# Kernel optimization log

Measured on AMD Instinct MI355X. Metric: run time of the kernel, lower is better.

## Reference

```python
import jax, jax.numpy as jnp
import numpy as np

B, S, H = 32, 1024, 1024

def setup_inputs() -> dict:
    key = jax.random.key(0)
    k1, k2, k3, k4, k5 = jax.random.split(key, 5)
    scale = 1.0 / np.sqrt(H)
    return {
        "decoder_hidden": jax.random.normal(k1, (B, H), jnp.float32),
        "encoder_outputs": jax.random.normal(k2, (B, S, H), jnp.float32),
        "U_w": jax.random.normal(k3, (H, H), jnp.float32) * scale,
        "W_w": jax.random.normal(k4, (H, H), jnp.float32) * scale,
        "v_w": jax.random.normal(k5, (H,), jnp.float32) * scale,
    }

def reference(decoder_hidden, encoder_outputs, U_w, W_w, v_w):
    # U(decoder_hidden): [B, H] @ [H, H]^T -> [B, H], broadcast over S
    U_h = jnp.einsum('bh,oh->bo', decoder_hidden, U_w)          # [B, H]
    W_s = jnp.einsum('bsh,oh->bso', encoder_outputs, W_w)       # [B, S, H]
    # v(tanh(U_h + W_s)) -> attention scores [B, S]
    att = jnp.einsum('bsh,h->bs', jnp.tanh(U_h[:, None, :] + W_s), v_w)
    alpha = jax.nn.softmax(att, axis=1)                          # [B, S]
    context = jnp.einsum('bs,bsh->bh', alpha, encoder_outputs)   # [B, H]
    return (context, alpha)
```

## Files before the change

### kernel.cpp

```cpp
#include <hip/hip_runtime.h>
#include <hip/hip_bf16.h>
#include <cstdint>
#include <cstddef>

#define B_DIM 32
#define S_DIM 1024
#define H_DIM 1024
#define M_DIM (B_DIM * S_DIM)

typedef __attribute__((ext_vector_type(8))) short bf16x8;
typedef __attribute__((ext_vector_type(4))) float f32x4;

static __device__ __forceinline__ unsigned short f2bf(float f) {
  unsigned u = __float_as_uint(f);
  u = (u + 0x7FFFu + ((u >> 16) & 1u)) >> 16;
  return (unsigned short)u;
}
static __device__ __forceinline__ float bf2f(unsigned short u) {
  return __uint_as_float(((unsigned)u) << 16);
}
static __device__ __forceinline__ float fast_tanh(float x) {
  return 1.f - 2.f / (__expf(2.f * x) + 1.f);
}

static __device__ __forceinline__ void gload16(const unsigned short* g, char* l) {
  __builtin_amdgcn_global_load_lds(
      (const __attribute__((address_space(1))) unsigned int*)g,
      (__attribute__((address_space(3))) unsigned int*)l, 16, 0, 0);
}

__global__ void k_prep_all(const float* __restrict__ E, unsigned short* __restrict__ Eb,
                           const float* __restrict__ W, unsigned short* __restrict__ Wb,
                           const float* __restrict__ dh, const float* __restrict__ Uw,
                           float* __restrict__ Uh) {
  const int bid = blockIdx.x;
  if (bid < 2048) {
    const int n8 = M_DIM * (H_DIM / 8);
    const int stride = 2048 * 256;
    for (int idx = bid * 256 + threadIdx.x; idx < n8; idx += stride) {
      const float4* gp = (const float4*)(E + (size_t)idx * 8);
      float4 lo = gp[0], hi = gp[1];
      bf16x8 w;
      w[0] = (short)f2bf(lo.x); w[1] = (short)f2bf(lo.y);
      w[2] = (short)f2bf(lo.z); w[3] = (short)f2bf(lo.w);
      w[4] = (short)f2bf(hi.x); w[5] = (short)f2bf(hi.y);
      w[6] = (short)f2bf(hi.z); w[7] = (short)f2bf(hi.w);
      *(bf16x8*)(Eb + (size_t)idx * 8) = w;
    }
  } else if (bid < 3072) {
    const int idx = (bid - 2048) * 256 + threadIdx.x;
    float4 v = ((const float4*)W)[idx];
    ushort4 o;
    o.x = f2bf(v.x); o.y = f2bf(v.y); o.z = f2bf(v.z); o.w = f2bf(v.w);
    ((ushort4*)Wb)[idx] = o;
  } else {
    const int wave = threadIdx.x >> 6;
    const int lane = threadIdx.x & 63;
    const int o = (bid - 3072) * 4 + wave;
    float uw[16];
#pragma unroll
    for (int k = 0; k < 16; ++k) uw[k] = Uw[o * H_DIM + k * 64 + lane];
    for (int b = 0; b < B_DIM; ++b) {
      float acc = 0.f;
#pragma unroll
      for (int k = 0; k < 16; ++k) acc += uw[k] * dh[b * H_DIM + k * 64 + lane];
#pragma unroll
      for (int msk = 32; msk >= 1; msk >>= 1) acc += __shfl_xor(acc, msk, 64);
      if (lane == 0) Uh[b * H_DIM + o] = acc;
    }
  }
}

#define A5_BM 256
#define A5_BN 256
#define A5_BUF 65536
#define NT_FAST 4

__launch_bounds__(512, 2)
__global__ void k_att6(const unsigned short* __restrict__ Eb,
                       const unsigned short* __restrict__ Wb,
                       const float* __restrict__ Uh,
                       const float* __restrict__ vw,
                       float* __restrict__ att_p) {
  __shared__ __align__(16) char lds[2 * A5_BUF];

  const int bid = blockIdx.x;
  const int xj = bid & 7;
  const int q  = bid >> 3;
  const int n_tile = q & 3;
  const int m_tile = ((q >> 2) << 3) | xj;
  const int m0 = m_tile * A5_BM;
  const int n0 = n_tile * A5_BN;
  const int b  = m0 >> 10;

  const int tid  = threadIdx.x;
  const int wid  = tid >> 6;
  const int lane = tid & 63;
  const int wm = (wid >> 2) * 128;
  const int wn = (wid & 3) * 64;

  size_t offA[4], offB[4];
  int ldsA[4], ldsB[4];
#pragma unroll
  for (int j = 0; j < 4; ++j) {
    const int chunk = j * 512 + tid;
    const int r  = chunk >> 3;
    const int c8 = (chunk & 7) ^ (r & 7);
    offA[j] = (size_t)(m0 + r) * H_DIM + c8 * 8;
    offB[j] = (size_t)(n0 + r) * H_DIM + c8 * 8;
    ldsA[j] = j * 8192 + wid * 1024;
    ldsB[j] = 32768 + j * 8192 + wid * 1024;
  }

  auto stage = [&](int t) {
    char* dst = lds + (t & 1) * A5_BUF;
    const size_t k0 = (size_t)t * 64;
#pragma unroll
    for (int j = 0; j < 4; ++j) gload16(Eb + offA[j] + k0, dst + ldsA[j]);
#pragma unroll
    for (int j = 0; j < 4; ++j) gload16(Wb + offB[j] + k0, dst + ldsB[j]);
  };

  const int fr_row = lane & 15;
  const int fr_k8  = lane >> 4;

  f32x4 acc[8][4];
#pragma unroll
  for (int mf = 0; mf < 8; ++mf)
#pragma unroll
    for (int nf = 0; nf < 4; ++nf) acc[mf][nf] = (f32x4)(0.0f);

  stage(0);

  for (int t = 0; t < 16; ++t) {
    asm volatile("s_waitcnt vmcnt(0)" ::: "memory");
    __builtin_amdgcn_s_barrier();
    asm volatile("" ::: "memory");

    if (t < 15) stage(t + 1);

    const char* As = lds + (t & 1) * A5_BUF;
    const char* Bs = As + 32768;

#pragma unroll
    for (int kh = 0; kh < 2; ++kh) {
      const int kb = kh * 32 + fr_k8 * 8;
      bf16x8 af[8], bfr[4];
#pragma unroll
      for (int mf = 0; mf < 8; ++mf) {
        const int row = wm + mf * 16 + fr_row;
        const int addr = (row * 128 + kb * 2) ^ ((row & 7) << 4);
        af[mf] = *(const bf16x8*)(As + addr);
      }
#pragma unroll
      for (int nf = 0; nf < 4; ++nf) {
        const int row = wn + nf * 16 + fr_row;
        const int addr = (row * 128 + kb * 2) ^ ((row & 7) << 4);
        bfr[nf] = *(const bf16x8*)(Bs + addr);
      }
      __builtin_amdgcn_s_setprio(1);
#pragma unroll
      for (int mf = 0; mf < 8; ++mf)
#pragma unroll
        for (int nf = 0; nf < 4; ++nf)
          acc[mf][nf] = __builtin_amdgcn_mfma_f32_16x16x32_bf16(af[mf], bfr[nf], acc[mf][nf], 0, 0, 0);
      __builtin_amdgcn_s_setprio(0);
    }
  }

  float* red = (float*)lds;

  const int col = lane & 15;
  const int rhi = lane >> 4;
  float uh[4], vv[4];
#pragma unroll
  for (int nf = 0; nf < 4; ++nf) {
    const int o = n0 + wn + nf * 16 + col;
    uh[nf] = Uh[b * H_DIM + o];
    vv[nf] = vw[o];
  }
#pragma unroll
  for (int mf = 0; mf < 8; ++mf) {
    float rs[4];
#pragma unroll
    for (int jj = 0; jj < 4; ++jj) {
      float s = 0.f;
#pragma unroll
      for (int nf = 0; nf < 4; ++nf) {
        const float x = acc[mf][nf][jj] + uh[nf];
        s += fast_tanh(x) * vv[nf];
      }
      rs[jj] = s;
    }
#pragma unroll
    for (int msk = 1; msk < 16; msk <<= 1) {
#pragma unroll
      for (int jj = 0; jj < 4; ++jj) rs[jj] += __shfl_xor(rs[jj], msk, 64);
    }
    if (col == 0) {
#pragma unroll
      for (int jj = 0; jj < 4; ++jj) {
        const int local = mf * 16 + rhi * 4 + jj;
        red[wid * 128 + local] = rs[jj];
      }
    }
  }
  __syncthreads();
  if (tid < 256) {
    const int mhalf = tid >> 7;
    const int loc = tid & 127;
    float sum = 0.f;
#pragma unroll
    for (int j = 0; j < 4; ++j) sum += red[(mhalf * 4 + j) * 128 + loc];
    att_p[(size_t)n_tile * M_DIM + m0 + tid] = sum;
  }
}

__global__ void k_ctx_sm(const unsigned short* __restrict__ Eb,
                         const float* __restrict__ att_p,
                         float* __restrict__ alpha_out,
                         float* __restrict__ ctx_p) {
  const int bid = blockIdx.x;
  const int b  = bid >> 2;
  const int sq = bid & 3;
  const int tid = threadIdx.x;
  __shared__ float red[8];
  __shared__ float qa[256];

  float a[4];
  float mx = -1e30f;
#pragma unroll
  for (int i = 0; i < 4; ++i) {
    const int s = i * 256 + tid;
    float v = 0.f;
#pragma unroll
    for (int t = 0; t < NT_FAST; ++t) v += att_p[(size_t)t * M_DIM + b * S_DIM + s];
    a[i] = v;
    mx = fmaxf(mx, v);
  }
#pragma unroll
  for (int msk = 32; msk >= 1; msk >>= 1) mx = fmaxf(mx, __shfl_xor(mx, msk, 64));
  if ((tid & 63) == 0) red[tid >> 6] = mx;
  __syncthreads();
  mx = fmaxf(fmaxf(red[0], red[1]), fmaxf(red[2], red[3]));
  float sum = 0.f;
#pragma unroll
  for (int i = 0; i < 4; ++i) { a[i] = __expf(a[i] - mx); sum += a[i]; }
#pragma unroll
  for (int msk = 32; msk >= 1; msk >>= 1) sum += __shfl_xor(sum, msk, 64);
  if ((tid & 63) == 0) red[4 + (tid >> 6)] = sum;
  __syncthreads();
  const float inv = 1.f / (red[4] + red[5] + red[6] + red[7]);
  if (sq == 0) {
#pragma unroll
    for (int i = 0; i < 4; ++i) alpha_out[b * S_DIM + i * 256 + tid] = a[i] * inv;
  }
  qa[tid] = a[sq] * inv;
  __syncthreads();

  const int h = tid * 4;
  const unsigned short* ep = Eb + (size_t)b * S_DIM * H_DIM + (size_t)(sq * 256) * H_DIM + h;
  float4 acc = make_float4(0.f, 0.f, 0.f, 0.f);
  for (int s = 0; s < 256; ++s) {
    const float al = qa[s];
    ushort4 v = *(const ushort4*)(ep + (size_t)s * H_DIM);
    acc.x += al * bf2f(v.x);
    acc.y += al * bf2f(v.y);
    acc.z += al * bf2f(v.z);
    acc.w += al * bf2f(v.w);
  }
  *(float4*)&ctx_p[(size_t)sq * (B_DIM * H_DIM) + b * H_DIM + h] = acc;
}

__global__ void k_ctx_reduce(const float* __restrict__ ctx_p, float* __restrict__ ctx) {
  const int i = blockIdx.x * 256 + threadIdx.x;
  ctx[i] = ctx_p[i] + ctx_p[32768 + i] + ctx_p[65536 + i] + ctx_p[98304 + i];
}

extern "C" void kernel_launch(void* const* d_in, const int* in_sizes, int n_in,
                              void* d_out, int out_size, void* d_ws, size_t ws_size,
                              hipStream_t stream) {
  (void)in_sizes; (void)n_in; (void)out_size; (void)ws_size;
  const float* dh  = (const float*)d_in[0];
  const float* enc = (const float*)d_in[1];
  const float* Uw  = (const float*)d_in[2];
  const float* Ww  = (const float*)d_in[3];
  const float* vw  = (const float*)d_in[4];
  float* ctx_out = (float*)d_out;
  float* alpha   = (float*)d_out + M_DIM;

  char* ws = (char*)d_ws;
  const size_t EB_BYTES = (size_t)M_DIM * H_DIM * 2;

  unsigned short* Eb = (unsigned short*)ws;
  unsigned short* Wb = (unsigned short*)(ws + EB_BYTES);
  float* Uh    = (float*)(ws + EB_BYTES + (2u << 20));
  float* att_p = (float*)(ws + EB_BYTES + (2u << 20) + (128u << 10));
  float* ctx_p = (float*)(ws + EB_BYTES + (2u << 20) + (128u << 10) + (1u << 20));

  k_prep_all<<<3328, 256, 0, stream>>>(enc, Eb, Ww, Wb, dh, Uw, Uh);
  k_att6<<<512, 512, 0, stream>>>(Eb, Wb, Uh, vw, att_p);
  k_ctx_sm<<<128, 256, 0, stream>>>(Eb, att_p, alpha, ctx_p);
  k_ctx_reduce<<<128, 256, 0, stream>>>(ctx_p, ctx_out);
}
```

Before: 139.8 us.

## Interleave GEMM K-loop into four barrier-separated phases and rebalance prep blocks

```diff
diff --git a/kernel.cpp b/kernel.cpp
--- a/kernel.cpp
+++ b/kernel.cpp
@@ -34,10 +34,33 @@
                            const float* __restrict__ dh, const float* __restrict__ Uw,
                            float* __restrict__ Uh) {
   const int bid = blockIdx.x;
-  if (bid < 2048) {
+  if (bid < 1024) {
+    const int wave = threadIdx.x >> 6;
+    const int lane = threadIdx.x & 63;
+    const int o = bid;
+    float uw[16];
+#pragma unroll
+    for (int k = 0; k < 16; ++k) uw[k] = Uw[o * H_DIM + k * 64 + lane];
+#pragma unroll
+    for (int bb = 0; bb < 8; ++bb) {
+      const int b = wave * 8 + bb;
+      float acc = 0.f;
+#pragma unroll
+      for (int k = 0; k < 16; ++k) acc += uw[k] * dh[b * H_DIM + k * 64 + lane];
+#pragma unroll
+      for (int msk = 32; msk >= 1; msk >>= 1) acc += __shfl_xor(acc, msk, 64);
+      if (lane == 0) Uh[b * H_DIM + o] = acc;
+    }
+  } else if (bid < 2048) {
+    const int idx = (bid - 1024) * 256 + threadIdx.x;
+    float4 v = ((const float4*)W)[idx];
+    ushort4 o;
+    o.x = f2bf(v.x); o.y = f2bf(v.y); o.z = f2bf(v.z); o.w = f2bf(v.w);
+    ((ushort4*)Wb)[idx] = o;
+  } else {
     const int n8 = M_DIM * (H_DIM / 8);
     const int stride = 2048 * 256;
-    for (int idx = bid * 256 + threadIdx.x; idx < n8; idx += stride) {
+    for (int idx = (bid - 2048) * 256 + threadIdx.x; idx < n8; idx += stride) {
       const float4* gp = (const float4*)(E + (size_t)idx * 8);
       float4 lo = gp[0], hi = gp[1];
       bf16x8 w;
@@ -47,27 +70,6 @@
       w[6] = (short)f2bf(hi.z); w[7] = (short)f2bf(hi.w);
       *(bf16x8*)(Eb + (size_t)idx * 8) = w;
     }
-  } else if (bid < 3072) {
-    const int idx = (bid - 2048) * 256 + threadIdx.x;
-    float4 v = ((const float4*)W)[idx];
-    ushort4 o;
-    o.x = f2bf(v.x); o.y = f2bf(v.y); o.z = f2bf(v.z); o.w = f2bf(v.w);
-    ((ushort4*)Wb)[idx] = o;
-  } else {
-    const int wave = threadIdx.x >> 6;
-    const int lane = threadIdx.x & 63;
-    const int o = (bid - 3072) * 4 + wave;
-    float uw[16];
-#pragma unroll
-    for (int k = 0; k < 16; ++k) uw[k] = Uw[o * H_DIM + k * 64 + lane];
-    for (int b = 0; b < B_DIM; ++b) {
-      float acc = 0.f;
-#pragma unroll
-      for (int k = 0; k < 16; ++k) acc += uw[k] * dh[b * H_DIM + k * 64 + lane];
-#pragma unroll
-      for (int msk = 32; msk >= 1; msk >>= 1) acc += __shfl_xor(acc, msk, 64);
-      if (lane == 0) Uh[b * H_DIM + o] = acc;
-    }
   }
 }
 
@@ -76,8 +78,11 @@
 #define A5_BUF 65536
 #define NT_FAST 4
 
+#define LDFRAG(base, row, kh) \
+  (*(const bf16x8*)((base) + ((((row) * 128) + ((kh) * 32 + fr_k8 * 8) * 2) ^ (((row) & 7) << 4))))
+
 __launch_bounds__(512, 2)
-__global__ void k_att6(const unsigned short* __restrict__ Eb,
+__global__ void k_att7(const unsigned short* __restrict__ Eb,
                        const unsigned short* __restrict__ Wb,
                        const float* __restrict__ Uh,
                        const float* __restrict__ vw,
@@ -112,15 +117,6 @@
     ldsB[j] = 32768 + j * 8192 + wid * 1024;
   }
 
-  auto stage = [&](int t) {
-    char* dst = lds + (t & 1) * A5_BUF;
-    const size_t k0 = (size_t)t * 64;
-#pragma unroll
-    for (int j = 0; j < 4; ++j) gload16(Eb + offA[j] + k0, dst + ldsA[j]);
-#pragma unroll
-    for (int j = 0; j < 4; ++j) gload16(Wb + offB[j] + k0, dst + ldsB[j]);
-  };
-
   const int fr_row = lane & 15;
   const int fr_k8  = lane >> 4;
 
@@ -130,42 +126,115 @@
 #pragma unroll
     for (int nf = 0; nf < 4; ++nf) acc[mf][nf] = (f32x4)(0.0f);
 
-  stage(0);
+  {
+    char* dst = lds;
+#pragma unroll
+    for (int j = 0; j < 4; ++j) gload16(Eb + offA[j], dst + ldsA[j]);
+#pragma unroll
+    for (int j = 0; j < 4; ++j) gload16(Wb + offB[j], dst + ldsB[j]);
+  }
 
   for (int t = 0; t < 16; ++t) {
     asm volatile("s_waitcnt vmcnt(0)" ::: "memory");
     __builtin_amdgcn_s_barrier();
     asm volatile("" ::: "memory");
 
-    if (t < 15) stage(t + 1);
-
     const char* As = lds + (t & 1) * A5_BUF;
     const char* Bs = As + 32768;
-
-#pragma unroll
-    for (int kh = 0; kh < 2; ++kh) {
-      const int kb = kh * 32 + fr_k8 * 8;
-      bf16x8 af[8], bfr[4];
-#pragma unroll
-      for (int mf = 0; mf < 8; ++mf) {
-        const int row = wm + mf * 16 + fr_row;
-        const int addr = (row * 128 + kb * 2) ^ ((row & 7) << 4);
-        af[mf] = *(const bf16x8*)(As + addr);
-      }
-#pragma unroll
-      for (int nf = 0; nf < 4; ++nf) {
-        const int row = wn + nf * 16 + fr_row;
-        const int addr = (row * 128 + kb * 2) ^ ((row & 7) << 4);
-        bfr[nf] = *(const bf16x8*)(Bs + addr);
-      }
-      __builtin_amdgcn_s_setprio(1);
-#pragma unroll
-      for (int mf = 0; mf < 8; ++mf)
-#pragma unroll
-        for (int nf = 0; nf < 4; ++nf)
-          acc[mf][nf] = __builtin_amdgcn_mfma_f32_16x16x32_bf16(af[mf], bfr[nf], acc[mf][nf], 0, 0, 0);
-      __builtin_amdgcn_s_setprio(0);
-    }
+    char* dst = lds + ((t + 1) & 1) * A5_BUF;
+    const size_t k1 = (size_t)(t + 1) * 64;
+    const bool st = (t < 15);
+
+    bf16x8 afl[8], afh[8], b01[4], b23[4], b01b[4];
+
+#pragma unroll
+    for (int mf = 0; mf < 4; ++mf) {
+      afl[mf * 2 + 0] = LDFRAG(As, wm + mf * 16 + fr_row, 0);
+      afl[mf * 2 + 1] = LDFRAG(As, wm + mf * 16 + fr_row, 1);
+    }
+#pragma unroll
+    for (int nf = 0; nf < 2; ++nf) {
+      b01[nf * 2 + 0] = LDFRAG(Bs, wn + nf * 16 + fr_row, 0);
+      b01[nf * 2 + 1] = LDFRAG(Bs, wn + nf * 16 + fr_row, 1);
+    }
+    if (st) { gload16(Eb + offA[0] + k1, dst + ldsA[0]);
+              gload16(Eb + offA[1] + k1, dst + ldsA[1]); }
+    __builtin_amdgcn_s_barrier();
+    asm volatile("s_waitcnt lgkmcnt(0)" ::: "memory");
+    __builtin_amdgcn_sched_barrier(0);
+    __builtin_amdgcn_s_setprio(1);
+#pragma unroll
+    for (int mf = 0; mf < 4; ++mf)
+#pragma unroll
+      for (int nf = 0; nf < 2; ++nf) {
+        acc[mf][nf] = __builtin_amdgcn_mfma_f32_16x16x32_bf16(afl[mf*2+0], b01[nf*2+0], acc[mf][nf], 0, 0, 0);
+        acc[mf][nf] = __builtin_amdgcn_mfma_f32_16x16x32_bf16(afl[mf*2+1], b01[nf*2+1], acc[mf][nf], 0, 0, 0);
+      }
+    __builtin_amdgcn_s_setprio(0);
+    __builtin_amdgcn_s_barrier();
+
+#pragma unroll
+    for (int nf = 0; nf < 2; ++nf) {
+      b23[nf * 2 + 0] = LDFRAG(Bs, wn + (nf + 2) * 16 + fr_row, 0);
+      b23[nf * 2 + 1] = LDFRAG(Bs, wn + (nf + 2) * 16 + fr_row, 1);
+    }
+    if (st) { gload16(Eb + offA[2] + k1, dst + ldsA[2]);
+              gload16(Eb + offA[3] + k1, dst + ldsA[3]); }
+    __builtin_amdgcn_s_barrier();
+    asm volatile("s_waitcnt lgkmcnt(0)" ::: "memory");
+    __builtin_amdgcn_sched_barrier(0);
+    __builtin_amdgcn_s_setprio(1);
+#pragma unroll
+    for (int mf = 0; mf < 4; ++mf)
+#pragma unroll
+      for (int nf = 0; nf < 2; ++nf) {
+        acc[mf][nf+2] = __builtin_amdgcn_mfma_f32_16x16x32_bf16(afl[mf*2+0], b23[nf*2+0], acc[mf][nf+2], 0, 0, 0);
+        acc[mf][nf+2] = __builtin_amdgcn_mfma_f32_16x16x32_bf16(afl[mf*2+1], b23[nf*2+1], acc[mf][nf+2], 0, 0, 0);
+      }
+    __builtin_amdgcn_s_setprio(0);
+    __builtin_amdgcn_s_barrier();
+
+#pragma unroll
+    for (int mf = 0; mf < 4; ++mf) {
+      afh[mf * 2 + 0] = LDFRAG(As, wm + (mf + 4) * 16 + fr_row, 0);
+      afh[mf * 2 + 1] = LDFRAG(As, wm + (mf + 4) * 16 + fr_row, 1);
+    }
+    if (st) { gload16(Wb + offB[0] + k1, dst + ldsB[0]);
+              gload16(Wb + offB[1] + k1, dst + ldsB[1]); }
+    __builtin_amdgcn_s_barrier();
+    asm volatile("s_waitcnt lgkmcnt(0)" ::: "memory");
+    __builtin_amdgcn_sched_barrier(0);
+    __builtin_amdgcn_s_setprio(1);
+#pragma unroll
+    for (int mf = 0; mf < 4; ++mf)
+#pragma unroll
+      for (int nf = 0; nf < 2; ++nf) {
+        acc[mf+4][nf+2] = __builtin_amdgcn_mfma_f32_16x16x32_bf16(afh[mf*2+0], b23[nf*2+0], acc[mf+4][nf+2], 0, 0, 0);
+        acc[mf+4][nf+2] = __builtin_amdgcn_mfma_f32_16x16x32_bf16(afh[mf*2+1], b23[nf*2+1], acc[mf+4][nf+2], 0, 0, 0);
+      }
+    __builtin_amdgcn_s_setprio(0);
+    __builtin_amdgcn_s_barrier();
+
+#pragma unroll
+    for (int nf = 0; nf < 2; ++nf) {
+      b01b[nf * 2 + 0] = LDFRAG(Bs, wn + nf * 16 + fr_row, 0);
+      b01b[nf * 2 + 1] = LDFRAG(Bs, wn + nf * 16 + fr_row, 1);
+    }
+    if (st) { gload16(Wb + offB[2] + k1, dst + ldsB[2]);
+              gload16(Wb + offB[3] + k1, dst + ldsB[3]); }
+    __builtin_amdgcn_s_barrier();
+    asm volatile("s_waitcnt lgkmcnt(0)" ::: "memory");
+    __builtin_amdgcn_sched_barrier(0);
+    __builtin_amdgcn_s_setprio(1);
+#pragma unroll
+    for (int mf = 0; mf < 4; ++mf)
+#pragma unroll
+      for (int nf = 0; nf < 2; ++nf) {
+        acc[mf+4][nf] = __builtin_amdgcn_mfma_f32_16x16x32_bf16(afh[mf*2+0], b01b[nf*2+0], acc[mf+4][nf], 0, 0, 0);
+        acc[mf+4][nf] = __builtin_amdgcn_mfma_f32_16x16x32_bf16(afh[mf*2+1], b01b[nf*2+1], acc[mf+4][nf], 0, 0, 0);
+      }
+    __builtin_amdgcn_s_setprio(0);
+    __builtin_amdgcn_s_barrier();
   }
 
   float* red = (float*)lds;
@@ -298,8 +367,8 @@
   float* att_p = (float*)(ws + EB_BYTES + (2u << 20) + (128u << 10));
   float* ctx_p = (float*)(ws + EB_BYTES + (2u << 20) + (128u << 10) + (1u << 20));
 
-  k_prep_all<<<3328, 256, 0, stream>>>(enc, Eb, Ww, Wb, dh, Uw, Uh);
-  k_att6<<<512, 512, 0, stream>>>(Eb, Wb, Uh, vw, att_p);
+  k_prep_all<<<4096, 256, 0, stream>>>(enc, Eb, Ww, Wb, dh, Uw, Uh);
+  k_att7<<<512, 512, 0, stream>>>(Eb, Wb, Uh, vw, att_p);
   k_ctx_sm<<<128, 256, 0, stream>>>(Eb, att_p, alpha, ctx_p);
   k_ctx_reduce<<<128, 256, 0, stream>>>(ctx_p, ctx_out);
 }
```

Result: faster. 132.6 us (-5.1%).

## Shrink GEMM tiles to 128x256 with k32 stages and reorder prep blocks

Applied to the files above, without the earlier changes.

```diff
diff --git a/kernel.cpp b/kernel.cpp
--- a/kernel.cpp
+++ b/kernel.cpp
@@ -34,10 +34,33 @@
                            const float* __restrict__ dh, const float* __restrict__ Uw,
                            float* __restrict__ Uh) {
   const int bid = blockIdx.x;
-  if (bid < 2048) {
+  if (bid < 1024) {
+    const int wave = threadIdx.x >> 6;
+    const int lane = threadIdx.x & 63;
+    const int o = bid;
+    float uw[16];
+#pragma unroll
+    for (int k = 0; k < 16; ++k) uw[k] = Uw[o * H_DIM + k * 64 + lane];
+#pragma unroll
+    for (int bb = 0; bb < 8; ++bb) {
+      const int b = wave * 8 + bb;
+      float acc = 0.f;
+#pragma unroll
+      for (int k = 0; k < 16; ++k) acc += uw[k] * dh[b * H_DIM + k * 64 + lane];
+#pragma unroll
+      for (int msk = 32; msk >= 1; msk >>= 1) acc += __shfl_xor(acc, msk, 64);
+      if (lane == 0) Uh[b * H_DIM + o] = acc;
+    }
+  } else if (bid < 2048) {
+    const int idx = (bid - 1024) * 256 + threadIdx.x;
+    float4 v = ((const float4*)W)[idx];
+    ushort4 o;
+    o.x = f2bf(v.x); o.y = f2bf(v.y); o.z = f2bf(v.z); o.w = f2bf(v.w);
+    ((ushort4*)Wb)[idx] = o;
+  } else {
     const int n8 = M_DIM * (H_DIM / 8);
     const int stride = 2048 * 256;
-    for (int idx = bid * 256 + threadIdx.x; idx < n8; idx += stride) {
+    for (int idx = (bid - 2048) * 256 + threadIdx.x; idx < n8; idx += stride) {
       const float4* gp = (const float4*)(E + (size_t)idx * 8);
       float4 lo = gp[0], hi = gp[1];
       bf16x8 w;
@@ -47,125 +70,99 @@
       w[6] = (short)f2bf(hi.z); w[7] = (short)f2bf(hi.w);
       *(bf16x8*)(Eb + (size_t)idx * 8) = w;
     }
-  } else if (bid < 3072) {
-    const int idx = (bid - 2048) * 256 + threadIdx.x;
-    float4 v = ((const float4*)W)[idx];
-    ushort4 o;
-    o.x = f2bf(v.x); o.y = f2bf(v.y); o.z = f2bf(v.z); o.w = f2bf(v.w);
-    ((ushort4*)Wb)[idx] = o;
-  } else {
-    const int wave = threadIdx.x >> 6;
-    const int lane = threadIdx.x & 63;
-    const int o = (bid - 3072) * 4 + wave;
-    float uw[16];
-#pragma unroll
-    for (int k = 0; k < 16; ++k) uw[k] = Uw[o * H_DIM + k * 64 + lane];
-    for (int b = 0; b < B_DIM; ++b) {
-      float acc = 0.f;
-#pragma unroll
-      for (int k = 0; k < 16; ++k) acc += uw[k] * dh[b * H_DIM + k * 64 + lane];
-#pragma unroll
-      for (int msk = 32; msk >= 1; msk >>= 1) acc += __shfl_xor(acc, msk, 64);
-      if (lane == 0) Uh[b * H_DIM + o] = acc;
-    }
-  }
-}
-
-#define A5_BM 256
-#define A5_BN 256
-#define A5_BUF 65536
+  }
+}
+
+#define A8_BM 128
+#define A8_BN 256
+#define A8_BUF 24576
 #define NT_FAST 4
 
-__launch_bounds__(512, 2)
-__global__ void k_att6(const unsigned short* __restrict__ Eb,
+#define LDFRAG32(base, row) \
+  (*(const bf16x8*)((base) + (((row) * 64 + fr_k8 * 16) ^ (((row) & 3) << 4))))
+
+__launch_bounds__(512, 4)
+__global__ void k_att8(const unsigned short* __restrict__ Eb,
                        const unsigned short* __restrict__ Wb,
                        const float* __restrict__ Uh,
                        const float* __restrict__ vw,
                        float* __restrict__ att_p) {
-  __shared__ __align__(16) char lds[2 * A5_BUF];
+  __shared__ __align__(16) char lds[2 * A8_BUF];
 
   const int bid = blockIdx.x;
   const int xj = bid & 7;
   const int q  = bid >> 3;
   const int n_tile = q & 3;
   const int m_tile = ((q >> 2) << 3) | xj;
-  const int m0 = m_tile * A5_BM;
-  const int n0 = n_tile * A5_BN;
+  const int m0 = m_tile * A8_BM;
+  const int n0 = n_tile * A8_BN;
   const int b  = m0 >> 10;
 
   const int tid  = threadIdx.x;
   const int wid  = tid >> 6;
   const int lane = tid & 63;
-  const int wm = (wid >> 2) * 128;
+  const int wm = (wid >> 2) * 64;
   const int wn = (wid & 3) * 64;
 
-  size_t offA[4], offB[4];
-  int ldsA[4], ldsB[4];
-#pragma unroll
-  for (int j = 0; j < 4; ++j) {
+  size_t offA0, offB[2];
+  int ldsA0, ldsB[2];
+  {
+    const int r  = tid >> 2;
+    const int c8 = (tid & 3) ^ (r & 3);
+    offA0 = (size_t)(m0 + r) * H_DIM + c8 * 8;
+    ldsA0 = wid * 1024;
+  }
+#pragma unroll
+  for (int j = 0; j < 2; ++j) {
     const int chunk = j * 512 + tid;
-    const int r  = chunk >> 3;
-    const int c8 = (chunk & 7) ^ (r & 7);
-    offA[j] = (size_t)(m0 + r) * H_DIM + c8 * 8;
+    const int r  = chunk >> 2;
+    const int c8 = (chunk & 3) ^ (r & 3);
     offB[j] = (size_t)(n0 + r) * H_DIM + c8 * 8;
-    ldsA[j] = j * 8192 + wid * 1024;
-    ldsB[j] = 32768 + j * 8192 + wid * 1024;
+    ldsB[j] = 8192 + j * 8192 + wid * 1024;
   }
 
   auto stage = [&](int t) {
-    char* dst = lds + (t & 1) * A5_BUF;
-    const size_t k0 = (size_t)t * 64;
-#pragma unroll
-    for (int j = 0; j < 4; ++j) gload16(Eb + offA[j] + k0, dst + ldsA[j]);
-#pragma unroll
-    for (int j = 0; j < 4; ++j) gload16(Wb + offB[j] + k0, dst + ldsB[j]);
+    char* dst = lds + (t & 1) * A8_BUF;
+    const size_t k0 = (size_t)t * 32;
+    gload16(Eb + offA0 + k0, dst + ldsA0);
+    gload16(Wb + offB[0] + k0, dst + ldsB[0]);
+    gload16(Wb + offB[1] + k0, dst + ldsB[1]);
   };
 
   const int fr_row = lane & 15;
   const int fr_k8  = lane >> 4;
 
-  f32x4 acc[8][4];
-#pragma unroll
-  for (int mf = 0; mf < 8; ++mf)
+  f32x4 acc[4][4];
+#pragma unroll
+  for (int mf = 0; mf < 4; ++mf)
 #pragma unroll
     for (int nf = 0; nf < 4; ++nf) acc[mf][nf] = (f32x4)(0.0f);
 
   stage(0);
 
-  for (int t = 0; t < 16; ++t) {
+  for (int t = 0; t < 32; ++t) {
     asm volatile("s_waitcnt vmcnt(0)" ::: "memory");
     __builtin_amdgcn_s_barrier();
     asm volatile("" ::: "memory");
 
-    if (t < 15) stage(t + 1);
-
-    const char* As = lds + (t & 1) * A5_BUF;
-    const char* Bs = As + 32768;
-
-#pragma unroll
-    for (int kh = 0; kh < 2; ++kh) {
-      const int kb = kh * 32 + fr_k8 * 8;
-      bf16x8 af[8], bfr[4];
-#pragma unroll
-      for (int mf = 0; mf < 8; ++mf) {
-        const int row = wm + mf * 16 + fr_row;
-        const int addr = (row * 128 + kb * 2) ^ ((row & 7) << 4);
-        af[mf] = *(const bf16x8*)(As + addr);
-      }
-#pragma unroll
-      for (int nf = 0; nf < 4; ++nf) {
-        const int row = wn + nf * 16 + fr_row;
-        const int addr = (row * 128 + kb * 2) ^ ((row & 7) << 4);
-        bfr[nf] = *(const bf16x8*)(Bs + addr);
-      }
-      __builtin_amdgcn_s_setprio(1);
-#pragma unroll
-      for (int mf = 0; mf < 8; ++mf)
-#pragma unroll
-        for (int nf = 0; nf < 4; ++nf)
-          acc[mf][nf] = __builtin_amdgcn_mfma_f32_16x16x32_bf16(af[mf], bfr[nf], acc[mf][nf], 0, 0, 0);
-      __builtin_amdgcn_s_setprio(0);
-    }
+    if (t < 31) stage(t + 1);
+
+    const char* As = lds + (t & 1) * A8_BUF;
+    const char* Bs = As + 8192;
+
+    bf16x8 af[4], bfr[4];
+#pragma unroll
+    for (int mf = 0; mf < 4; ++mf) af[mf] = LDFRAG32(As, wm + mf * 16 + fr_row);
+#pragma unroll
+    for (int nf = 0; nf < 4; ++nf) bfr[nf] = LDFRAG32(Bs, wn + nf * 16 + fr_row);
+
+    __builtin_amdgcn_s_setprio(1);
+#pragma unroll
+    for (int mf = 0; mf < 4; ++mf)
+#pragma unroll
+      for (int nf = 0; nf < 4; ++nf)
+        acc[mf][nf] = __builtin_amdgcn_mfma_f32_16x16x32_bf16(af[mf], bfr[nf], acc[mf][nf], 0, 0, 0);
+    __builtin_amdgcn_s_setprio(0);
   }
 
   float* red = (float*)lds;
@@ -180,7 +177,7 @@
     vv[nf] = vw[o];
   }
 #pragma unroll
-  for (int mf = 0; mf < 8; ++mf) {
+  for (int mf = 0; mf < 4; ++mf) {
     float rs[4];
 #pragma unroll
     for (int jj = 0; jj < 4; ++jj) {
@@ -201,17 +198,17 @@
 #pragma unroll
       for (int jj = 0; jj < 4; ++jj) {
         const int local = mf * 16 + rhi * 4 + jj;
-        red[wid * 128 + local] = rs[jj];
+        red[wid * 64 + local] = rs[jj];
       }
     }
   }
   __syncthreads();
-  if (tid < 256) {
-    const int mhalf = tid >> 7;
-    const int loc = tid & 127;
+  if (tid < 128) {
+    const int h4 = (tid >> 6) * 4;
+    const int loc = tid & 63;
     float sum = 0.f;
 #pragma unroll
-    for (int j = 0; j < 4; ++j) sum += red[(mhalf * 4 + j) * 128 + loc];
+    for (int j = 0; j < 4; ++j) sum += red[(h4 + j) * 64 + loc];
     att_p[(size_t)n_tile * M_DIM + m0 + tid] = sum;
   }
 }
@@ -298,8 +295,8 @@
   float* att_p = (float*)(ws + EB_BYTES + (2u << 20) + (128u << 10));
   float* ctx_p = (float*)(ws + EB_BYTES + (2u << 20) + (128u << 10) + (1u << 20));
 
-  k_prep_all<<<3328, 256, 0, stream>>>(enc, Eb, Ww, Wb, dh, Uw, Uh);
-  k_att6<<<512, 512, 0, stream>>>(Eb, Wb, Uh, vw, att_p);
+  k_prep_all<<<4096, 256, 0, stream>>>(enc, Eb, Ww, Wb, dh, Uw, Uh);
+  k_att8<<<1024, 512, 0, stream>>>(Eb, Wb, Uh, vw, att_p);
   k_ctx_sm<<<128, 256, 0, stream>>>(Eb, att_p, alpha, ctx_p);
   k_ctx_reduce<<<128, 256, 0, stream>>>(ctx_p, ctx_out);
 }
```

Result: no change. 137.4 us (-1.7%).
